# Optimization experiments

Hardware: AMD Instinct MI355X
Metric: run time of the kernel (lower is better)

The kernel has to match this reference:

```python
import jax, jax.numpy as jnp
import numpy as np
from jax import lax

DEPTH_SIZE = 16


def _conv2d(x, w, b):
    # x: [B,C,H,W], w: [O,I,5,5], 'SAME' == padding=2 for k=5
    y = lax.conv_general_dilated(x, w, (1, 1), 'SAME',
                                 dimension_numbers=('NCHW', 'OIHW', 'NCHW'))
    return y + b[None, :, None, None]


def _bn(x, g, b, m, v):
    # eval-mode BatchNorm2d, eps=1e-5
    scale = g / jnp.sqrt(v + 1e-5)
    return (x - m[None, :, None, None]) * scale[None, :, None, None] + b[None, :, None, None]


def setup_inputs() -> dict:
    key = jax.random.key(0)
    ks = jax.random.split(key, 24)
    f32 = jnp.float32
    B, H, W = 1, 384, 384

    def cw(k, shape):
        fan_in = float(np.prod(shape[1:]))
        return jax.random.normal(k, shape, f32) / np.float32(np.sqrt(fan_in))

    inp = {
        'light':     jax.random.uniform(ks[0], (B, 3, H, W), f32),
        'albedo':    jax.random.uniform(ks[1], (B, 3, H, W), f32),
        'normals':   jax.random.normal(ks[2], (B, 3, H, W), f32),
        'positions': jax.random.normal(ks[3], (B, 3, H, W), f32),
        'c1_w': cw(ks[4], (32, 9, 5, 5)),  'c1_b': jnp.zeros((32,), f32),
        'bn1_g': jax.random.uniform(ks[5], (32,), f32, 0.5, 1.5),
        'bn1_b': jax.random.normal(ks[6], (32,), f32) * 0.1,
        'bn1_m': jax.random.normal(ks[7], (32,), f32) * 0.1,
        'bn1_v': jax.random.uniform(ks[8], (32,), f32, 0.5, 1.5),
        'c2_w': cw(ks[9], (8, 32, 5, 5)),  'c2_b': jnp.zeros((8,), f32),
        'bn2_g': jax.random.uniform(ks[10], (8,), f32, 0.5, 1.5),
        'bn2_b': jax.random.normal(ks[11], (8,), f32) * 0.1,
        'bn2_m': jax.random.normal(ks[12], (8,), f32) * 0.1,
        'bn2_v': jax.random.uniform(ks[13], (8,), f32, 0.5, 1.5),
        'c3_w': cw(ks[14], (1, 8, 5, 5)),  'c3_b': jnp.zeros((1,), f32),
        'bn3_g': jax.random.uniform(ks[15], (1,), f32, 0.5, 1.5),
        'bn3_b': jax.random.normal(ks[16], (1,), f32) * 0.1,
        'bn3_m': jax.random.normal(ks[17], (1,), f32) * 0.1,
        'bn3_v': jax.random.uniform(ks[18], (1,), f32, 0.5, 1.5),
        'f_w': cw(ks[19], (4, 4, 7, 7, 7)),
        # weight-channel bias = 1 keeps the divide-by-weight well conditioned
        'f_b': jnp.concatenate([jnp.zeros((3,), f32), jnp.ones((1,), f32)]),
    }
    return inp


def reference(light, albedo, normals, positions,
              c1_w, c1_b, bn1_g, bn1_b, bn1_m, bn1_v,
              c2_w, c2_b, bn2_g, bn2_b, bn2_m, bn2_v,
              c3_w, c3_b, bn3_g, bn3_b, bn3_m, bn3_v,
              f_w, f_b):
    D = DEPTH_SIZE
    B, _, H, W = light.shape

    # estimate_depth CNN on cat(light, albedo, normals) -> sigmoid embedding in (0,1)
    x = jnp.concatenate([light, albedo, normals], axis=1)           # [B,9,H,W]
    h = jax.nn.relu(_bn(_conv2d(x, c1_w, c1_b), bn1_g, bn1_b, bn1_m, bn1_v))
    h = jax.nn.relu(_bn(_conv2d(h, c2_w, c2_b), bn2_g, bn2_b, bn2_m, bn2_v))
    emb = jax.nn.sigmoid(_bn(_conv2d(h, c3_w, c3_b), bn3_g, bn3_b, bn3_m, bn3_v))  # [B,1,H,W]

    # quantize depth into bin index (long() == floor for positive values)
    depth = jnp.floor(emb[:, 0] * (D - 1e-5)).astype(jnp.int32)     # [B,H,W], in [0,15]

    # project: scatter per-pixel (light, 1) into the 16-slot depth volume
    wl = jnp.concatenate([light, jnp.ones((B, 1, H, W), light.dtype)], axis=1)   # [B,4,H,W]
    onehot = (depth[:, None, :, :] == jnp.arange(D)[None, :, None, None]).astype(light.dtype)  # [B,D,H,W]
    vol = wl[:, :, None, :, :] * onehot[:, None, :, :, :]           # [B,4,D,H,W]

    # dense 7^3 Conv3d filter, padding=3 == 'SAME'
    fvol = lax.conv_general_dilated(vol, f_w, (1, 1, 1), 'SAME',
                                    dimension_numbers=('NCDHW', 'OIDHW', 'NCDHW'))
    fvol = fvol + f_b[None, :, None, None, None]                    # [B,4,D,H,W]

    # unproject: gather back at each pixel's depth bin
    idx = jnp.broadcast_to(depth[:, None, None, :, :], (B, 4, 1, H, W))
    gathered = jnp.take_along_axis(fvol, idx, axis=2)[:, :, 0]      # [B,4,H,W]

    filtered_light, weight = gathered[:, :3], gathered[:, 3:4]
    return (filtered_light / weight) * albedo                       # [B,3,H,W]
```

## Files before the change

### kernel.cpp

```cpp
#include <hip/hip_runtime.h>
#include <math.h>

#define HW 384
#define PLANE (HW*HW)

#define WT1_OFF   0
#define SC1_OFF   7296
#define SH1_OFF   7328
#define WT2_OFF   7360
#define SC2_OFF   13760
#define SH2_OFF   13768
#define W3_OFF    13776
#define SC3_OFF   13976
#define SH3_OFF   13977
#define FWT_OFF   13984
#define H1_OFF    32768
#define H2_OFF    (32768 + 32*PLANE)
#define DEPTH_OFF (32768 + 64*PLANE)

__global__ void prep_kernel(
    const float* __restrict__ c1w, const float* __restrict__ c1b,
    const float* __restrict__ g1, const float* __restrict__ b1,
    const float* __restrict__ m1, const float* __restrict__ v1,
    const float* __restrict__ c2w, const float* __restrict__ c2b,
    const float* __restrict__ g2, const float* __restrict__ b2,
    const float* __restrict__ m2, const float* __restrict__ v2,
    const float* __restrict__ c3w, const float* __restrict__ c3b,
    const float* __restrict__ g3, const float* __restrict__ b3,
    const float* __restrict__ m3, const float* __restrict__ v3,
    const float* __restrict__ fw, float* __restrict__ W)
{
    int gid = blockIdx.x * 256 + threadIdx.x;
    int gstr = gridDim.x * 256;
    for (int i = gid; i < 7200; i += gstr) {
        int w = i / 1800, r = i % 1800;
        int ct = r >> 3, o = r & 7;
        int oc = w * 8 + o;
        W[WT1_OFF + i] = c1w[oc * 225 + ct];
    }
    for (int i = gid; i < 6400; i += gstr) {
        int gw = i / 400, r = i % 400;
        int cc2 = r / 200, r2 = r % 200, tap = r2 >> 3, o = r2 & 7;
        int cab = (gw >> 2) * 8 + (gw & 3) * 2 + cc2;
        W[WT2_OFF + i] = c2w[o * 800 + cab * 25 + tap];
    }
    for (int i = gid; i < 6860; i += gstr) {
        int s = i / 20, k = i % 20;
        float v = 0.f;
        if (k < 16) { int o = k >> 2, c = k & 3; v = fw[o * 1372 + c * 343 + s]; }
        W[FWT_OFF + i] = v;
    }
    if (blockIdx.x == 0) {
        int tid = threadIdx.x;
        if (tid < 32) {
            float sc = g1[tid] / sqrtf(v1[tid] + 1e-5f);
            W[SC1_OFF + tid] = sc;
            W[SH1_OFF + tid] = (c1b[tid] - m1[tid]) * sc + b1[tid];
        }
        if (tid < 8) {
            float sc = g2[tid] / sqrtf(v2[tid] + 1e-5f);
            W[SC2_OFF + tid] = sc;
            W[SH2_OFF + tid] = (c2b[tid] - m2[tid]) * sc + b2[tid];
        }
        if (tid < 200) W[W3_OFF + tid] = c3w[tid];
        if (tid == 0) {
            float sc = g3[0] / sqrtf(v3[0] + 1e-5f);
            W[SC3_OFF] = sc;
            W[SH3_OFF] = (c3b[0] - m3[0]) * sc + b3[0];
        }
    }
}

__global__ __launch_bounds__(256, 4) void conv1_kernel(
    const float* __restrict__ light, const float* __restrict__ albedo,
    const float* __restrict__ normals, const float* __restrict__ W,
    float* __restrict__ h1)
{
    __shared__ __align__(16) float tile[9 * 432];
    int tid = threadIdx.x;
    int wu = __builtin_amdgcn_readfirstlane(tid >> 6);
    int slot = tid & 63;
    int qx = slot & 7, ty = slot >> 3;
    int bx = blockIdx.x % 12, by = blockIdx.x / 12;
    int x0 = bx * 32, y0 = by * 8;

    for (int p = tid; p < 432; p += 256) {
        int py = p / 36, px = p % 36;
        int gy = y0 + py - 2, gx = x0 + px - 2;
        bool ok = ((unsigned)gy < (unsigned)HW) && ((unsigned)gx < (unsigned)HW);
        int gofs = ok ? (gy * HW + gx) : 0;
#pragma unroll
        for (int c = 0; c < 3; ++c) {
            float a = light[c * PLANE + gofs];
            float b = albedo[c * PLANE + gofs];
            float n = normals[c * PLANE + gofs];
            tile[(c    ) * 432 + p] = ok ? a : 0.f;
            tile[(c + 3) * 432 + p] = ok ? b : 0.f;
            tile[(c + 6) * 432 + p] = ok ? n : 0.f;
        }
    }
    __syncthreads();

    float acc[8][4];
#pragma unroll
    for (int o = 0; o < 8; ++o)
#pragma unroll
        for (int j = 0; j < 4; ++j) acc[o][j] = 0.f;

    const float* wbase = W + WT1_OFF + wu * 1800;
#pragma unroll 1
    for (int c = 0; c < 9; ++c) {
        const float* bc = tile + c * 432;
        const float* wc = wbase + c * 200;
#pragma unroll
        for (int ky = 0; ky < 5; ++ky) {
            const float* rp = bc + (ty + ky) * 36 + qx * 4;
            float4 ra = *(const float4*)rp;
            float4 rb = *(const float4*)(rp + 4);
            float row[8] = {ra.x, ra.y, ra.z, ra.w, rb.x, rb.y, rb.z, rb.w};
#pragma unroll
            for (int kx = 0; kx < 5; ++kx) {
                const float* wt = wc + (ky * 5 + kx) * 8;
                float4 wA = *(const float4*)wt;
                float4 wB = *(const float4*)(wt + 4);
#pragma unroll
                for (int j = 0; j < 4; ++j) {
                    float v = row[kx + j];
                    acc[0][j] = fmaf(v, wA.x, acc[0][j]);
                    acc[1][j] = fmaf(v, wA.y, acc[1][j]);
                    acc[2][j] = fmaf(v, wA.z, acc[2][j]);
                    acc[3][j] = fmaf(v, wA.w, acc[3][j]);
                    acc[4][j] = fmaf(v, wB.x, acc[4][j]);
                    acc[5][j] = fmaf(v, wB.y, acc[5][j]);
                    acc[6][j] = fmaf(v, wB.z, acc[6][j]);
                    acc[7][j] = fmaf(v, wB.w, acc[7][j]);
                }
            }
        }
    }

    int pix = (y0 + ty) * HW + x0 + qx * 4;
#pragma unroll
    for (int o = 0; o < 8; ++o) {
        int oc = wu * 8 + o;
        float sc = W[SC1_OFF + oc], sh = W[SH1_OFF + oc];
        float4 rv;
        rv.x = fmaxf(fmaf(acc[o][0], sc, sh), 0.f);
        rv.y = fmaxf(fmaf(acc[o][1], sc, sh), 0.f);
        rv.z = fmaxf(fmaf(acc[o][2], sc, sh), 0.f);
        rv.w = fmaxf(fmaf(acc[o][3], sc, sh), 0.f);
        *(float4*)&h1[oc * PLANE + pix] = rv;
    }
}

__global__ __launch_bounds__(256, 4) void conv2_kernel(
    const float* __restrict__ h1, const float* __restrict__ W,
    float* __restrict__ h2p)
{
    __shared__ __align__(16) float lds[4608];
    int tid = threadIdx.x;
    int wu = __builtin_amdgcn_readfirstlane(tid >> 6);
    int slot = tid & 63;
    int qx = slot & 7, ty = slot >> 3;
    int bid = blockIdx.x;
    int q = bid & 3, sp = bid >> 2;
    int bx = sp % 12, by = sp / 12;
    int x0 = bx * 32, y0 = by * 8;
    int cbase = q * 8;

    for (int p = tid; p < 432; p += 256) {
        int py = p / 36, px = p % 36;
        int gy = y0 + py - 2, gx = x0 + px - 2;
        bool ok = ((unsigned)gy < (unsigned)HW) && ((unsigned)gx < (unsigned)HW);
        int gofs = ok ? (gy * HW + gx) : 0;
#pragma unroll
        for (int cc = 0; cc < 8; ++cc) {
            float v = h1[(cbase + cc) * PLANE + gofs];
            lds[cc * 432 + p] = ok ? v : 0.f;
        }
    }
    __syncthreads();

    float acc[8][4];
#pragma unroll
    for (int o = 0; o < 8; ++o)
#pragma unroll
        for (int j = 0; j < 4; ++j) acc[o][j] = 0.f;

    int gw = q * 4 + wu;
#pragma unroll 1
    for (int cc2 = 0; cc2 < 2; ++cc2) {
        const float* bc = lds + (2 * wu + cc2) * 432;
        const float* wc = W + WT2_OFF + gw * 400 + cc2 * 200;
#pragma unroll
        for (int ky = 0; ky < 5; ++ky) {
            const float* rp = bc + (ty + ky) * 36 + qx * 4;
            float4 ra = *(const float4*)rp;
            float4 rb = *(const float4*)(rp + 4);
            float row[8] = {ra.x, ra.y, ra.z, ra.w, rb.x, rb.y, rb.z, rb.w};
#pragma unroll
            for (int kx = 0; kx < 5; ++kx) {
                const float* wt = wc + (ky * 5 + kx) * 8;
                float4 wA = *(const float4*)wt;
                float4 wB = *(const float4*)(wt + 4);
#pragma unroll
                for (int j = 0; j < 4; ++j) {
                    float v = row[kx + j];
                    acc[0][j] = fmaf(v, wA.x, acc[0][j]);
                    acc[1][j] = fmaf(v, wA.y, acc[1][j]);
                    acc[2][j] = fmaf(v, wA.z, acc[2][j]);
                    acc[3][j] = fmaf(v, wA.w, acc[3][j]);
                    acc[4][j] = fmaf(v, wB.x, acc[4][j]);
                    acc[5][j] = fmaf(v, wB.y, acc[5][j]);
                    acc[6][j] = fmaf(v, wB.z, acc[6][j]);
                    acc[7][j] = fmaf(v, wB.w, acc[7][j]);
                }
            }
        }
    }
    __syncthreads();

    if (wu >= 2) {
        float* pp = lds + (wu - 2) * 2304 + slot * 36;
#pragma unroll
        for (int o = 0; o < 8; ++o)
            *(float4*)(pp + o * 4) = make_float4(acc[o][0], acc[o][1], acc[o][2], acc[o][3]);
    }
    __syncthreads();
    if (wu < 2) {
        const float* pp = lds + wu * 2304 + slot * 36;
#pragma unroll
        for (int o = 0; o < 8; ++o) {
            float4 t = *(const float4*)(pp + o * 4);
            acc[o][0] += t.x; acc[o][1] += t.y; acc[o][2] += t.z; acc[o][3] += t.w;
        }
    }
    __syncthreads();
    if (wu == 1) {
        float* pp = lds + slot * 36;
#pragma unroll
        for (int o = 0; o < 8; ++o)
            *(float4*)(pp + o * 4) = make_float4(acc[o][0], acc[o][1], acc[o][2], acc[o][3]);
    }
    __syncthreads();
    if (wu == 0) {
        const float* pp = lds + slot * 36;
        int pix = (y0 + ty) * HW + x0 + qx * 4;
#pragma unroll
        for (int o = 0; o < 8; ++o) {
            float4 t = *(const float4*)(pp + o * 4);
            float4 rv;
            rv.x = acc[o][0] + t.x; rv.y = acc[o][1] + t.y;
            rv.z = acc[o][2] + t.z; rv.w = acc[o][3] + t.w;
            *(float4*)&h2p[(q * 8 + o) * PLANE + pix] = rv;
        }
    }
}

__global__ __launch_bounds__(256, 2) void conv3_kernel(
    const float* __restrict__ h2p, const float* __restrict__ W,
    int* __restrict__ depth)
{
    __shared__ float tile[8 * 432];
    int tid = threadIdx.x;
    int tx = tid & 31, ty = tid >> 5;
    int bx = blockIdx.x % 12, by = blockIdx.x / 12;
    int x0 = bx * 32 - 2, y0 = by * 8 - 2;

    for (int p = tid; p < 432; p += 256) {
        int py = p / 36, px = p % 36;
        int gy = y0 + py, gx = x0 + px;
        bool ok = ((unsigned)gy < (unsigned)HW) && ((unsigned)gx < (unsigned)HW);
        int gofs = ok ? (gy * HW + gx) : 0;
#pragma unroll
        for (int c = 0; c < 8; ++c) {
            float t = ((h2p[c * PLANE + gofs] + h2p[(c + 8) * PLANE + gofs])
                     + h2p[(c + 16) * PLANE + gofs]) + h2p[(c + 24) * PLANE + gofs];
            float r = fmaxf(fmaf(t, W[SC2_OFF + c], W[SH2_OFF + c]), 0.f);
            tile[c * 432 + p] = ok ? r : 0.f;
        }
    }
    __syncthreads();

    float a = 0.f;
#pragma unroll 1
    for (int c = 0; c < 8; ++c) {
#pragma unroll
        for (int ky = 0; ky < 5; ++ky) {
#pragma unroll
            for (int kx = 0; kx < 5; ++kx) {
                a = fmaf(tile[c * 432 + (ty + ky) * 36 + tx + kx],
                         W[W3_OFF + (c * 5 + ky) * 5 + kx], a);
            }
        }
    }
    float y = fmaf(a, W[SC3_OFF], W[SH3_OFF]);
    float s = 1.f / (1.f + expf(-y));
    int d = (int)floorf(s * (16.f - 1e-5f));

    int gy = by * 8 + ty, gx = bx * 32 + tx;
    depth[gy * HW + gx] = d;
}

__global__ __launch_bounds__(256, 2) void final_kernel(
    const float* __restrict__ light, const float* __restrict__ albedo,
    const float* __restrict__ W, const float* __restrict__ fb,
    float* __restrict__ out)
{
    __shared__ __align__(16) float fwl[6860];
    __shared__ float ltile[3][14][38];
    __shared__ int   dtile[14][38];

    int tid = threadIdx.x;
    int tx = tid & 31, ty = tid >> 5;
    int bx = blockIdx.x % 12, by = blockIdx.x / 12;
    int x0 = bx * 32 - 3, y0 = by * 8 - 3;

    for (int i = tid; i < 6860; i += 256) fwl[i] = W[FWT_OFF + i];

    const int* dmap = ((const int*)W) + DEPTH_OFF;
    for (int p = tid; p < 14 * 38; p += 256) {
        int py = p / 38, px = p % 38;
        int gy = y0 + py, gx = x0 + px;
        bool ok = ((unsigned)gy < (unsigned)HW) && ((unsigned)gx < (unsigned)HW);
        int gofs = ok ? (gy * HW + gx) : 0;
        int dv = dmap[gofs];
        dtile[py][px] = ok ? dv : -1000;
#pragma unroll
        for (int c = 0; c < 3; ++c) {
            float lv = light[c * PLANE + gofs];
            ltile[c][py][px] = ok ? lv : 0.f;
        }
    }
    __syncthreads();

    int d0 = dtile[ty + 3][tx + 3];
    float a0 = fb[0], a1 = fb[1], a2 = fb[2], a3 = fb[3];

#pragma unroll 1
    for (int dy = 0; dy < 7; ++dy) {
#pragma unroll
        for (int dx = 0; dx < 7; ++dx) {
            int dd = dtile[ty + dy][tx + dx];
            int dz = dd - d0 + 3;
            if ((unsigned)dz < 7u) {
                int s = (dz * 7 + dy) * 7 + dx;
                const float* fs = fwl + s * 20;
                float4 w0 = *(const float4*)(fs);
                float4 w1 = *(const float4*)(fs + 4);
                float4 w2 = *(const float4*)(fs + 8);
                float4 w3 = *(const float4*)(fs + 12);
                float l0 = ltile[0][ty + dy][tx + dx];
                float l1 = ltile[1][ty + dy][tx + dx];
                float l2 = ltile[2][ty + dy][tx + dx];
                a0 += l0 * w0.x + l1 * w0.y + l2 * w0.z + w0.w;
                a1 += l0 * w1.x + l1 * w1.y + l2 * w1.z + w1.w;
                a2 += l0 * w2.x + l1 * w2.y + l2 * w2.z + w2.w;
                a3 += l0 * w3.x + l1 * w3.y + l2 * w3.z + w3.w;
            }
        }
    }

    int gy = by * 8 + ty, gx = bx * 32 + tx;
    int pix = gy * HW + gx;
    out[0 * PLANE + pix] = a0 / a3 * albedo[0 * PLANE + pix];
    out[1 * PLANE + pix] = a1 / a3 * albedo[1 * PLANE + pix];
    out[2 * PLANE + pix] = a2 / a3 * albedo[2 * PLANE + pix];
}

extern "C" void kernel_launch(void* const* d_in, const int* in_sizes, int n_in,
                              void* d_out, int out_size, void* d_ws, size_t ws_size,
                              hipStream_t stream) {
    const float* light     = (const float*)d_in[0];
    const float* albedo    = (const float*)d_in[1];
    const float* normals   = (const float*)d_in[2];
    const float* c1_w = (const float*)d_in[4];
    const float* c1_b = (const float*)d_in[5];
    const float* bn1_g = (const float*)d_in[6];
    const float* bn1_b = (const float*)d_in[7];
    const float* bn1_m = (const float*)d_in[8];
    const float* bn1_v = (const float*)d_in[9];
    const float* c2_w = (const float*)d_in[10];
    const float* c2_b = (const float*)d_in[11];
    const float* bn2_g = (const float*)d_in[12];
    const float* bn2_b = (const float*)d_in[13];
    const float* bn2_m = (const float*)d_in[14];
    const float* bn2_v = (const float*)d_in[15];
    const float* c3_w = (const float*)d_in[16];
    const float* c3_b = (const float*)d_in[17];
    const float* bn3_g = (const float*)d_in[18];
    const float* bn3_b = (const float*)d_in[19];
    const float* bn3_m = (const float*)d_in[20];
    const float* bn3_v = (const float*)d_in[21];
    const float* f_w = (const float*)d_in[22];
    const float* f_b = (const float*)d_in[23];

    float* W = (float*)d_ws;
    float* h1 = W + H1_OFF;
    float* h2p = W + H2_OFF;
    int* depth = ((int*)d_ws) + DEPTH_OFF;
    float* out = (float*)d_out;

    hipLaunchKernelGGL(prep_kernel, dim3(16), dim3(256), 0, stream,
                       c1_w, c1_b, bn1_g, bn1_b, bn1_m, bn1_v,
                       c2_w, c2_b, bn2_g, bn2_b, bn2_m, bn2_v,
                       c3_w, c3_b, bn3_g, bn3_b, bn3_m, bn3_v,
                       f_w, W);
    hipLaunchKernelGGL(conv1_kernel, dim3(576), dim3(256), 0, stream,
                       light, albedo, normals, W, h1);
    hipLaunchKernelGGL(conv2_kernel, dim3(2304), dim3(256), 0, stream,
                       h1, W, h2p);
    hipLaunchKernelGGL(conv3_kernel, dim3(576), dim3(256), 0, stream,
                       h2p, W, depth);
    hipLaunchKernelGGL(final_kernel, dim3(576), dim3(256), 0, stream,
                       light, albedo, W, f_b, out);
}
```

Measured before the change: 95.93 us.

## Fuse conv3 depth computation into final filter kernel; split conv1 across 8 waves

Removes the separate conv3 kernel and its depth-map round trip. The final kernel now loads a halo-extended tile of the reduced conv2 partials, computes conv3, sigmoid and depth for its 14x38 region in shared memory, then reuses that buffer for the 3D filter weights. Conv1 moves to 512-thread blocks with 4 output channels per wave, which lowers register pressure and raises parallelism. In exchange, depth is recomputed redundantly in halo regions, and the fused kernel has extra syncs and higher shared-memory use.

Result: slower. 104.6 us (+9.0%).

```diff
diff --git a/kernel.cpp b/kernel.cpp
--- a/kernel.cpp
+++ b/kernel.cpp
@@ -16,7 +16,6 @@
 #define FWT_OFF   13984
 #define H1_OFF    32768
 #define H2_OFF    (32768 + 32*PLANE)
-#define DEPTH_OFF (32768 + 64*PLANE)
 
 __global__ void prep_kernel(
     const float* __restrict__ c1w, const float* __restrict__ c1b,
@@ -33,9 +32,9 @@
     int gid = blockIdx.x * 256 + threadIdx.x;
     int gstr = gridDim.x * 256;
     for (int i = gid; i < 7200; i += gstr) {
-        int w = i / 1800, r = i % 1800;
-        int ct = r >> 3, o = r & 7;
-        int oc = w * 8 + o;
+        int wu = i / 900, r = i % 900;
+        int ct = r >> 2, o = r & 3;
+        int oc = wu * 4 + o;
         W[WT1_OFF + i] = c1w[oc * 225 + ct];
     }
     for (int i = gid; i < 6400; i += gstr) {
@@ -71,7 +70,7 @@
     }
 }
 
-__global__ __launch_bounds__(256, 4) void conv1_kernel(
+__global__ __launch_bounds__(512, 4) void conv1_kernel(
     const float* __restrict__ light, const float* __restrict__ albedo,
     const float* __restrict__ normals, const float* __restrict__ W,
     float* __restrict__ h1)
@@ -84,7 +83,8 @@
     int bx = blockIdx.x % 12, by = blockIdx.x / 12;
     int x0 = bx * 32, y0 = by * 8;
 
-    for (int p = tid; p < 432; p += 256) {
+    if (tid < 432) {
+        int p = tid;
         int py = p / 36, px = p % 36;
         int gy = y0 + py - 2, gx = x0 + px - 2;
         bool ok = ((unsigned)gy < (unsigned)HW) && ((unsigned)gx < (unsigned)HW);
@@ -101,17 +101,17 @@
     }
     __syncthreads();
 
-    float acc[8][4];
-#pragma unroll
-    for (int o = 0; o < 8; ++o)
+    float acc[4][4];
+#pragma unroll
+    for (int o = 0; o < 4; ++o)
 #pragma unroll
         for (int j = 0; j < 4; ++j) acc[o][j] = 0.f;
 
-    const float* wbase = W + WT1_OFF + wu * 1800;
+    const float* wbase = W + WT1_OFF + wu * 900;
 #pragma unroll 1
     for (int c = 0; c < 9; ++c) {
         const float* bc = tile + c * 432;
-        const float* wc = wbase + c * 200;
+        const float* wc = wbase + c * 100;
 #pragma unroll
         for (int ky = 0; ky < 5; ++ky) {
             const float* rp = bc + (ty + ky) * 36 + qx * 4;
@@ -120,9 +120,7 @@
             float row[8] = {ra.x, ra.y, ra.z, ra.w, rb.x, rb.y, rb.z, rb.w};
 #pragma unroll
             for (int kx = 0; kx < 5; ++kx) {
-                const float* wt = wc + (ky * 5 + kx) * 8;
-                float4 wA = *(const float4*)wt;
-                float4 wB = *(const float4*)(wt + 4);
+                float4 wA = *(const float4*)(wc + (ky * 5 + kx) * 4);
 #pragma unroll
                 for (int j = 0; j < 4; ++j) {
                     float v = row[kx + j];
@@ -130,10 +128,6 @@
                     acc[1][j] = fmaf(v, wA.y, acc[1][j]);
                     acc[2][j] = fmaf(v, wA.z, acc[2][j]);
                     acc[3][j] = fmaf(v, wA.w, acc[3][j]);
-                    acc[4][j] = fmaf(v, wB.x, acc[4][j]);
-                    acc[5][j] = fmaf(v, wB.y, acc[5][j]);
-                    acc[6][j] = fmaf(v, wB.z, acc[6][j]);
-                    acc[7][j] = fmaf(v, wB.w, acc[7][j]);
                 }
             }
         }
@@ -141,8 +135,8 @@
 
     int pix = (y0 + ty) * HW + x0 + qx * 4;
 #pragma unroll
-    for (int o = 0; o < 8; ++o) {
-        int oc = wu * 8 + o;
+    for (int o = 0; o < 4; ++o) {
+        int oc = wu * 4 + o;
         float sc = W[SC1_OFF + oc], sh = W[SH1_OFF + oc];
         float4 rv;
         rv.x = fmaxf(fmaf(acc[o][0], sc, sh), 0.f);
@@ -257,57 +251,12 @@
     }
 }
 
-__global__ __launch_bounds__(256, 2) void conv3_kernel(
+__global__ __launch_bounds__(256, 4) void final_kernel(
+    const float* __restrict__ light, const float* __restrict__ albedo,
     const float* __restrict__ h2p, const float* __restrict__ W,
-    int* __restrict__ depth)
+    const float* __restrict__ fb, float* __restrict__ out)
 {
-    __shared__ float tile[8 * 432];
-    int tid = threadIdx.x;
-    int tx = tid & 31, ty = tid >> 5;
-    int bx = blockIdx.x % 12, by = blockIdx.x / 12;
-    int x0 = bx * 32 - 2, y0 = by * 8 - 2;
-
-    for (int p = tid; p < 432; p += 256) {
-        int py = p / 36, px = p % 36;
-        int gy = y0 + py, gx = x0 + px;
-        bool ok = ((unsigned)gy < (unsigned)HW) && ((unsigned)gx < (unsigned)HW);
-        int gofs = ok ? (gy * HW + gx) : 0;
-#pragma unroll
-        for (int c = 0; c < 8; ++c) {
-            float t = ((h2p[c * PLANE + gofs] + h2p[(c + 8) * PLANE + gofs])
-                     + h2p[(c + 16) * PLANE + gofs]) + h2p[(c + 24) * PLANE + gofs];
-            float r = fmaxf(fmaf(t, W[SC2_OFF + c], W[SH2_OFF + c]), 0.f);
-            tile[c * 432 + p] = ok ? r : 0.f;
-        }
-    }
-    __syncthreads();
-
-    float a = 0.f;
-#pragma unroll 1
-    for (int c = 0; c < 8; ++c) {
-#pragma unroll
-        for (int ky = 0; ky < 5; ++ky) {
-#pragma unroll
-            for (int kx = 0; kx < 5; ++kx) {
-                a = fmaf(tile[c * 432 + (ty + ky) * 36 + tx + kx],
-                         W[W3_OFF + (c * 5 + ky) * 5 + kx], a);
-            }
-        }
-    }
-    float y = fmaf(a, W[SC3_OFF], W[SH3_OFF]);
-    float s = 1.f / (1.f + expf(-y));
-    int d = (int)floorf(s * (16.f - 1e-5f));
-
-    int gy = by * 8 + ty, gx = bx * 32 + tx;
-    depth[gy * HW + gx] = d;
-}
-
-__global__ __launch_bounds__(256, 2) void final_kernel(
-    const float* __restrict__ light, const float* __restrict__ albedo,
-    const float* __restrict__ W, const float* __restrict__ fb,
-    float* __restrict__ out)
-{
-    __shared__ __align__(16) float fwl[6860];
+    __shared__ __align__(16) float u[6860];
     __shared__ float ltile[3][14][38];
     __shared__ int   dtile[14][38];
 
@@ -315,23 +264,61 @@
     int tx = tid & 31, ty = tid >> 5;
     int bx = blockIdx.x % 12, by = blockIdx.x / 12;
     int x0 = bx * 32 - 3, y0 = by * 8 - 3;
-
-    for (int i = tid; i < 6860; i += 256) fwl[i] = W[FWT_OFF + i];
-
-    const int* dmap = ((const int*)W) + DEPTH_OFF;
-    for (int p = tid; p < 14 * 38; p += 256) {
+    int x2 = x0 - 2, y2 = y0 - 2;
+
+    for (int p = tid; p < 756; p += 256) {
+        int r = p / 42, cpx = p % 42;
+        int gy = y2 + r, gx = x2 + cpx;
+        bool ok = ((unsigned)gy < (unsigned)HW) && ((unsigned)gx < (unsigned)HW);
+        int gofs = ok ? (gy * HW + gx) : 0;
+#pragma unroll
+        for (int c = 0; c < 8; ++c) {
+            float t = ((h2p[c * PLANE + gofs] + h2p[(c + 8) * PLANE + gofs])
+                     + h2p[(c + 16) * PLANE + gofs]) + h2p[(c + 24) * PLANE + gofs];
+            float rr = fmaxf(fmaf(t, W[SC2_OFF + c], W[SH2_OFF + c]), 0.f);
+            u[c * 756 + p] = ok ? rr : 0.f;
+        }
+    }
+    for (int p = tid; p < 532; p += 256) {
         int py = p / 38, px = p % 38;
         int gy = y0 + py, gx = x0 + px;
         bool ok = ((unsigned)gy < (unsigned)HW) && ((unsigned)gx < (unsigned)HW);
         int gofs = ok ? (gy * HW + gx) : 0;
-        int dv = dmap[gofs];
-        dtile[py][px] = ok ? dv : -1000;
 #pragma unroll
         for (int c = 0; c < 3; ++c) {
             float lv = light[c * PLANE + gofs];
             ltile[c][py][px] = ok ? lv : 0.f;
         }
     }
+    __syncthreads();
+
+    for (int p = tid; p < 532; p += 256) {
+        int py = p / 38, px = p % 38;
+        int gy = y0 + py, gx = x0 + px;
+        bool ok = ((unsigned)gy < (unsigned)HW) && ((unsigned)gx < (unsigned)HW);
+        int d = -1000;
+        if (ok) {
+            float a = 0.f;
+#pragma unroll 1
+            for (int c = 0; c < 8; ++c) {
+#pragma unroll
+                for (int ky = 0; ky < 5; ++ky) {
+#pragma unroll
+                    for (int kx = 0; kx < 5; ++kx) {
+                        a = fmaf(u[c * 756 + (py + ky) * 42 + (px + kx)],
+                                 W[W3_OFF + (c * 5 + ky) * 5 + kx], a);
+                    }
+                }
+            }
+            float y = fmaf(a, W[SC3_OFF], W[SH3_OFF]);
+            float s = 1.f / (1.f + expf(-y));
+            d = (int)floorf(s * (16.f - 1e-5f));
+        }
+        dtile[py][px] = d;
+    }
+    __syncthreads();
+
+    for (int i = tid; i < 6860; i += 256) u[i] = W[FWT_OFF + i];
     __syncthreads();
 
     int d0 = dtile[ty + 3][tx + 3];
@@ -345,7 +332,7 @@
             int dz = dd - d0 + 3;
             if ((unsigned)dz < 7u) {
                 int s = (dz * 7 + dy) * 7 + dx;
-                const float* fs = fwl + s * 20;
+                const float* fs = u + s * 20;
                 float4 w0 = *(const float4*)(fs);
                 float4 w1 = *(const float4*)(fs + 4);
                 float4 w2 = *(const float4*)(fs + 8);
@@ -398,7 +385,6 @@
     float* W = (float*)d_ws;
     float* h1 = W + H1_OFF;
     float* h2p = W + H2_OFF;
-    int* depth = ((int*)d_ws) + DEPTH_OFF;
     float* out = (float*)d_out;
 
     hipLaunchKernelGGL(prep_kernel, dim3(16), dim3(256), 0, stream,
@@ -406,12 +392,10 @@
                        c2_w, c2_b, bn2_g, bn2_b, bn2_m, bn2_v,
                        c3_w, c3_b, bn3_g, bn3_b, bn3_m, bn3_v,
                        f_w, W);
-    hipLaunchKernelGGL(conv1_kernel, dim3(576), dim3(256), 0, stream,
+    hipLaunchKernelGGL(conv1_kernel, dim3(576), dim3(512), 0, stream,
                        light, albedo, normals, W, h1);
     hipLaunchKernelGGL(conv2_kernel, dim3(2304), dim3(256), 0, stream,
                        h1, W, h2p);
-    hipLaunchKernelGGL(conv3_kernel, dim3(576), dim3(256), 0, stream,
-                       h2p, W, depth);
     hipLaunchKernelGGL(final_kernel, dim3(576), dim3(256), 0, stream,
-                       light, albedo, W, f_b, out);
+                       light, albedo, h2p, W, f_b, out);
 }
```
